# Performance work log

Hardware: AMD Instinct MI355X
Metric: run time of the kernel (lower is better)

Reference implementation:

```python
import jax, jax.numpy as jnp
import numpy as np

SIZE = 1024
M = 10            # log2(SIZE); number of butterfly factors
N_TERMS = 10
BATCH = 8192

# diagonal offset of butterfly j (order matches torch: range(m)[::-1])
DIAGS = [1 << (M - 1 - j) for j in range(M)]


def setup_inputs() -> dict:
    key = jax.random.key(0)
    k1, k2, k3, k4, k5 = jax.random.split(key, 5)
    x = jax.random.normal(k1, (BATCH, SIZE), dtype=jnp.float32)
    diag = jax.random.normal(k2, (M, SIZE), dtype=jnp.float32)
    subpad = jax.random.normal(k3, (M, SIZE), dtype=jnp.float32)
    suppad = jax.random.normal(k4, (M, SIZE), dtype=jnp.float32)
    logit = jax.random.normal(k5, (N_TERMS, M), dtype=jnp.float32)
    # zero the padded positions: subdiag has length SIZE-d stored in [d:],
    # superdiag has length SIZE-d stored in [:-d]
    idx = np.arange(SIZE)
    sub_mask = np.stack([idx >= d for d in DIAGS]).astype(np.float32)
    sup_mask = np.stack([idx < SIZE - d for d in DIAGS]).astype(np.float32)
    subpad = subpad * jnp.asarray(sub_mask)
    suppad = suppad * jnp.asarray(sup_mask)
    return {"x": x, "diag": diag, "subpad": subpad, "suppad": suppad, "logit": logit}


def _butterfly(x, dg, sb, sp, d):
    # out = dg*x; out[d:] += subdiag*x[:-d]; out[:-d] += superdiag*x[d:]
    z = jnp.zeros(x.shape[:-1] + (d,), x.dtype)
    x_right = jnp.concatenate([z, x[..., :-d]], axis=-1)  # x shifted right by d
    x_left = jnp.concatenate([x[..., d:], z], axis=-1)    # x shifted left by d
    return dg * x + sb * x_right + sp * x_left


def reference(x, diag, subpad, suppad, logit):
    prob = jax.nn.softmax(logit, axis=-1)  # (n_terms, m)
    out = x
    for i in range(N_TERMS)[::-1]:
        # apply all m butterflies to current output, stack on last dim
        ys = jnp.stack(
            [_butterfly(out, diag[j], subpad[j], suppad[j], DIAGS[j]) for j in range(M)],
            axis=-1,
        )  # (..., size, m)
        out = jnp.einsum('bsm,m->bs', ys, prob[i])
    return out
```

## Files before the change

### kernel.cpp

```cpp
#include <hip/hip_runtime.h>

#define SIZE 1024
#define MM 10
#define NTERMS 10

typedef _Float16 f16;
typedef __attribute__((ext_vector_type(8))) _Float16 f16x8;
typedef __attribute__((ext_vector_type(4))) _Float16 f16x4;
typedef __attribute__((ext_vector_type(4))) float    f32x4;
typedef __attribute__((ext_vector_type(2))) int      i2;

__device__ __forceinline__ float4 ldq(const float* p) { return *(const float4*)p; }

#define FMA4F(W, v0, v1, v2, v3)                                     \
    a0 = fmaf((W)[0], (v0), a0); a1 = fmaf((W)[1], (v1), a1);        \
    a2 = fmaf((W)[2], (v2), a2); a3 = fmaf((W)[3], (v3), a3);

__global__ __launch_bounds__(256, 2)
void precompute_G(const float* __restrict__ diag,
                  const float* __restrict__ subpad,
                  const float* __restrict__ suppad,
                  const float* __restrict__ logit,
                  float* __restrict__ G)
{
    __shared__ float buf[2][2][SIZE];

    const int tid = threadIdx.x;
    const int s0  = tid * 4;
    const int rowbase = blockIdx.x * 2;

    #pragma unroll
    for (int r = 0; r < 2; ++r) {
        float4 v;
        v.x = (rowbase + r == s0 + 0) ? 1.f : 0.f;
        v.y = (rowbase + r == s0 + 1) ? 1.f : 0.f;
        v.z = (rowbase + r == s0 + 2) ? 1.f : 0.f;
        v.w = (rowbase + r == s0 + 3) ? 1.f : 0.f;
        *(float4*)&buf[0][r][s0] = v;
    }
    __syncthreads();

    int cur = 0;
    for (int t = 0; t < NTERMS; ++t) {
        const int i = NTERMS - 1 - t;

        float lg[MM];
        float mx = -3.4e38f;
        #pragma unroll
        for (int j = 0; j < MM; ++j) { lg[j] = logit[i * MM + j]; mx = fmaxf(mx, lg[j]); }
        float ssum = 0.f;
        #pragma unroll
        for (int j = 0; j < MM; ++j) { lg[j] = __expf(lg[j] - mx); ssum += lg[j]; }
        const float inv = 1.0f / ssum;

        float D[4] = {0.f, 0.f, 0.f, 0.f};
        float Wsb[MM][4], Wsp[MM][4];
        #pragma unroll
        for (int j = 0; j < MM; ++j) {
            const float pj = lg[j] * inv;
            const float4 dg = ldq(diag   + j * SIZE + s0);
            const float4 sb = ldq(subpad + j * SIZE + s0);
            const float4 sp = ldq(suppad + j * SIZE + s0);
            D[0] = fmaf(pj, dg.x, D[0]); D[1] = fmaf(pj, dg.y, D[1]);
            D[2] = fmaf(pj, dg.z, D[2]); D[3] = fmaf(pj, dg.w, D[3]);
            Wsb[j][0] = pj * sb.x; Wsb[j][1] = pj * sb.y;
            Wsb[j][2] = pj * sb.z; Wsb[j][3] = pj * sb.w;
            Wsp[j][0] = pj * sp.x; Wsp[j][1] = pj * sp.y;
            Wsp[j][2] = pj * sp.z; Wsp[j][3] = pj * sp.w;
        }

        const bool last = (t == NTERMS - 1);
        for (int r = 0; r < 2; ++r) {
            const float* row = &buf[cur][r][0];

            const float4 xo = ldq(row + s0);
            float a0 = D[0] * xo.x, a1 = D[1] * xo.y,
                  a2 = D[2] * xo.z, a3 = D[3] * xo.w;

            const float4 xl = ldq(row + (s0 >= 4         ? s0 - 4 : 0));
            const float4 xr = ldq(row + (s0 + 4 <= 1020  ? s0 + 4 : 1020));

            FMA4F(Wsb[9], xl.w, xo.x, xo.y, xo.z)
            FMA4F(Wsp[9], xo.y, xo.z, xo.w, xr.x)
            FMA4F(Wsb[8], xl.z, xl.w, xo.x, xo.y)
            FMA4F(Wsp[8], xo.z, xo.w, xr.x, xr.y)
            FMA4F(Wsb[7], xl.x, xl.y, xl.z, xl.w)
            FMA4F(Wsp[7], xr.x, xr.y, xr.z, xr.w)
            #pragma unroll
            for (int j = 0; j <= 6; ++j) {
                const int d = 512 >> j;
                const float4 xm = ldq(row + (s0 >= d        ? s0 - d : 0));
                const float4 xp = ldq(row + (s0 + d <= 1020 ? s0 + d : 1020));
                FMA4F(Wsb[j], xm.x, xm.y, xm.z, xm.w)
                FMA4F(Wsp[j], xp.x, xp.y, xp.z, xp.w)
            }

            if (last) {
                *(float4*)(G + (long)(rowbase + r) * SIZE + s0) =
                    make_float4(a0, a1, a2, a3);
            } else {
                *(float4*)&buf[cur ^ 1][r][s0] = make_float4(a0, a1, a2, a3);
            }
        }
        __syncthreads();
        cur ^= 1;
    }
}

__global__ __launch_bounds__(256)
void transpose_cast(const float* __restrict__ G, f16* __restrict__ Gt)
{
    __shared__ float tile[64][65];
    const int tid = threadIdx.x;
    const int k0 = blockIdx.x * 64;
    const int s0 = blockIdx.y * 64;
    const int rr = tid >> 4;
    const int cc = (tid & 15) * 4;

    #pragma unroll
    for (int p = 0; p < 4; ++p) {
        const float4 v = ldq(G + (long)(k0 + rr + p * 16) * SIZE + s0 + cc);
        *(float4*)&tile[rr + p * 16][cc] = v;
    }
    __syncthreads();
    #pragma unroll
    for (int p = 0; p < 4; ++p) {
        const int s = rr + p * 16;
        f16x4 h;
        h[0] = (f16)tile[cc + 0][s];
        h[1] = (f16)tile[cc + 1][s];
        h[2] = (f16)tile[cc + 2][s];
        h[3] = (f16)tile[cc + 3][s];
        *(f16x4*)(Gt + (long)(s0 + s) * SIZE + k0 + cc) = h;
    }
}

#define BMT 128
#define BNT 128
#define BKT 32
#define PADK 40
#define NKT (1024 / BKT)

__device__ __forceinline__ void cvt16(const float4& v0, const float4& v1, f16x8& h) {
    h[0] = (f16)v0.x; h[1] = (f16)v0.y; h[2] = (f16)v0.z; h[3] = (f16)v0.w;
    h[4] = (f16)v1.x; h[5] = (f16)v1.y; h[6] = (f16)v1.z; h[7] = (f16)v1.w;
}

__global__ __launch_bounds__(256, 2)
void gemm_f16(const float* __restrict__ x,
              const f16* __restrict__ Gt,
              float* __restrict__ out)
{
    __shared__ f16 Xs[2][BMT][PADK];
    __shared__ f16 Gs[2][BNT][PADK];

    const int tid  = threadIdx.x;
    const int bm   = blockIdx.x >> 3;
    const int bn   = blockIdx.x & 7;
    const int w    = tid >> 6, lane = tid & 63;
    const int wm   = w >> 1,  wn   = w & 1;
    const int lr   = lane & 15, lk = lane >> 4;

    const int sr   = tid >> 1;
    const int sh16 = (tid & 1) * 16;
    const float* xrow = x  + (long)(bm * BMT + sr) * 1024 + sh16;
    const f16*   grow = Gt + (long)(bn * BNT + sr) * 1024 + sh16;

    f32x4 acc[4][4];
    #pragma unroll
    for (int mi = 0; mi < 4; ++mi)
        #pragma unroll
        for (int ni = 0; ni < 4; ++ni)
            acc[mi][ni] = (f32x4){0.f, 0.f, 0.f, 0.f};

    {
        const float4 v0 = ldq(xrow), v1 = ldq(xrow + 4),
                     v2 = ldq(xrow + 8), v3 = ldq(xrow + 12);
        const f16x8 g0 = *(const f16x8*)grow;
        const f16x8 g1 = *(const f16x8*)(grow + 8);
        f16x8 h0, h1; cvt16(v0, v1, h0); cvt16(v2, v3, h1);
        *(f16x8*)&Xs[0][sr][sh16]     = h0;
        *(f16x8*)&Xs[0][sr][sh16 + 8] = h1;
        *(f16x8*)&Gs[0][sr][sh16]     = g0;
        *(f16x8*)&Gs[0][sr][sh16 + 8] = g1;
    }
    __syncthreads();

    int cur = 0;
    for (int kt = 0; kt < NKT; ++kt) {
        float4 v0, v1, v2, v3; f16x8 g0, g1;
        const bool more = (kt + 1 < NKT);
        if (more) {
            const float* xp = xrow + (kt + 1) * BKT;
            const f16*   gp = grow + (kt + 1) * BKT;
            v0 = ldq(xp); v1 = ldq(xp + 4); v2 = ldq(xp + 8); v3 = ldq(xp + 12);
            g0 = *(const f16x8*)gp; g1 = *(const f16x8*)(gp + 8);
        }

        f16x8 a[4], b[4];
        #pragma unroll
        for (int mi = 0; mi < 4; ++mi)
            a[mi] = *(const f16x8*)&Xs[cur][wm * 64 + mi * 16 + lr][lk * 8];
        #pragma unroll
        for (int ni = 0; ni < 4; ++ni)
            b[ni] = *(const f16x8*)&Gs[cur][wn * 64 + ni * 16 + lr][lk * 8];
        #pragma unroll
        for (int mi = 0; mi < 4; ++mi)
            #pragma unroll
            for (int ni = 0; ni < 4; ++ni)
                acc[mi][ni] = __builtin_amdgcn_mfma_f32_16x16x32_f16(
                    a[mi], b[ni], acc[mi][ni], 0, 0, 0);

        if (more) {
            f16x8 h0, h1; cvt16(v0, v1, h0); cvt16(v2, v3, h1);
            *(f16x8*)&Xs[cur ^ 1][sr][sh16]     = h0;
            *(f16x8*)&Xs[cur ^ 1][sr][sh16 + 8] = h1;
            *(f16x8*)&Gs[cur ^ 1][sr][sh16]     = g0;
            *(f16x8*)&Gs[cur ^ 1][sr][sh16 + 8] = g1;
        }
        __syncthreads();
        cur ^= 1;
    }

    const long orow0 = (long)bm * BMT + wm * 64 + lk * 4;
    const int  ocol0 = bn * BNT + wn * 64 + lr;
    #pragma unroll
    for (int mi = 0; mi < 4; ++mi)
        #pragma unroll
        for (int ni = 0; ni < 4; ++ni)
            #pragma unroll
            for (int q = 0; q < 4; ++q)
                out[(orow0 + mi * 16 + q) * 1024 + ocol0 + ni * 16] = acc[mi][ni][q];
}

#define RPB 16
#define MIX_L(acc, r32, ww) \
    asm("v_fma_mix_f32 %0, %1, %2, %0 op_sel:[0,0,0] op_sel_hi:[1,0,0]" \
        : "+v"(acc) : "v"(r32), "v"(ww))
#define MIX_H(acc, r32, ww) \
    asm("v_fma_mix_f32 %0, %1, %2, %0 op_sel:[1,0,0] op_sel_hi:[1,0,0]" \
        : "+v"(acc) : "v"(r32), "v"(ww))

__global__ __launch_bounds__(256, 2)
void butterfly_h16mix(const float* __restrict__ x,
                      const float* __restrict__ diag,
                      const float* __restrict__ subpad,
                      const float* __restrict__ suppad,
                      const float* __restrict__ logit,
                      float* __restrict__ out)
{
    __shared__ f16 buf[2][RPB][SIZE];
    const int tid = threadIdx.x;
    const int s0  = tid * 4;
    const long rowbase = (long)blockIdx.x * RPB;

    #pragma unroll
    for (int r = 0; r < RPB; ++r) {
        const float4 v = ldq(x + (rowbase + r) * SIZE + s0);
        f16x4 h;
        h[0] = (f16)v.x; h[1] = (f16)v.y; h[2] = (f16)v.z; h[3] = (f16)v.w;
        *(f16x4*)&buf[0][r][s0] = h;
    }
    __syncthreads();

    int cur = 0;
    for (int t = 0; t < NTERMS; ++t) {
        const int i = NTERMS - 1 - t;
        float lg[MM];
        float mx = -3.4e38f;
        #pragma unroll
        for (int j = 0; j < MM; ++j) { lg[j] = logit[i * MM + j]; mx = fmaxf(mx, lg[j]); }
        float ssum = 0.f;
        #pragma unroll
        for (int j = 0; j < MM; ++j) { lg[j] = __expf(lg[j] - mx); ssum += lg[j]; }
        const float inv = 1.0f / ssum;

        float D[4] = {0.f, 0.f, 0.f, 0.f};
        float Wsb[MM][4], Wsp[MM][4];
        #pragma unroll
        for (int j = 0; j < MM; ++j) {
            const float pj = lg[j] * inv;
            const float4 dg = ldq(diag   + j * SIZE + s0);
            const float4 sb = ldq(subpad + j * SIZE + s0);
            const float4 sp = ldq(suppad + j * SIZE + s0);
            D[0] = fmaf(pj, dg.x, D[0]); D[1] = fmaf(pj, dg.y, D[1]);
            D[2] = fmaf(pj, dg.z, D[2]); D[3] = fmaf(pj, dg.w, D[3]);
            Wsb[j][0] = pj * sb.x; Wsb[j][1] = pj * sb.y;
            Wsb[j][2] = pj * sb.z; Wsb[j][3] = pj * sb.w;
            Wsp[j][0] = pj * sp.x; Wsp[j][1] = pj * sp.y;
            Wsp[j][2] = pj * sp.z; Wsp[j][3] = pj * sp.w;
        }

        const bool last = (t == NTERMS - 1);
        for (int r = 0; r < RPB; ++r) {
            const f16* row = &buf[cur][r][0];
            const i2 xo = *(const i2*)&row[s0];
            const i2 xl = *(const i2*)&row[(s0 >= 4)        ? s0 - 4 : 0];
            const i2 xr = *(const i2*)&row[(s0 + 4 <= 1020) ? s0 + 4 : 1020];
            float a0 = 0.f, a1 = 0.f, a2 = 0.f, a3 = 0.f;

            MIX_L(a0, xo.x, D[0]); MIX_H(a1, xo.x, D[1]);
            MIX_L(a2, xo.y, D[2]); MIX_H(a3, xo.y, D[3]);
            MIX_H(a0, xl.y, Wsb[9][0]); MIX_L(a1, xo.x, Wsb[9][1]);
            MIX_H(a2, xo.x, Wsb[9][2]); MIX_L(a3, xo.y, Wsb[9][3]);
            MIX_H(a0, xo.x, Wsp[9][0]); MIX_L(a1, xo.y, Wsp[9][1]);
            MIX_H(a2, xo.y, Wsp[9][2]); MIX_L(a3, xr.x, Wsp[9][3]);
            MIX_L(a0, xl.y, Wsb[8][0]); MIX_H(a1, xl.y, Wsb[8][1]);
            MIX_L(a2, xo.x, Wsb[8][2]); MIX_H(a3, xo.x, Wsb[8][3]);
            MIX_L(a0, xo.y, Wsp[8][0]); MIX_H(a1, xo.y, Wsp[8][1]);
            MIX_L(a2, xr.x, Wsp[8][2]); MIX_H(a3, xr.x, Wsp[8][3]);
            MIX_L(a0, xl.x, Wsb[7][0]); MIX_H(a1, xl.x, Wsb[7][1]);
            MIX_L(a2, xl.y, Wsb[7][2]); MIX_H(a3, xl.y, Wsb[7][3]);
            MIX_L(a0, xr.x, Wsp[7][0]); MIX_H(a1, xr.x, Wsp[7][1]);
            MIX_L(a2, xr.y, Wsp[7][2]); MIX_H(a3, xr.y, Wsp[7][3]);
            #pragma unroll
            for (int j = 0; j <= 6; ++j) {
                const int d = 512 >> j;
                const i2 xm = *(const i2*)&row[(s0 >= d)        ? s0 - d : 0];
                const i2 xp = *(const i2*)&row[(s0 + d <= 1020) ? s0 + d : 1020];
                MIX_L(a0, xm.x, Wsb[j][0]); MIX_H(a1, xm.x, Wsb[j][1]);
                MIX_L(a2, xm.y, Wsb[j][2]); MIX_H(a3, xm.y, Wsb[j][3]);
                MIX_L(a0, xp.x, Wsp[j][0]); MIX_H(a1, xp.x, Wsp[j][1]);
                MIX_L(a2, xp.y, Wsp[j][2]); MIX_H(a3, xp.y, Wsp[j][3]);
            }

            if (last) {
                *(float4*)(out + (rowbase + r) * SIZE + s0) =
                    make_float4(a0, a1, a2, a3);
            } else {
                f16x4 hv;
                hv[0] = (f16)a0; hv[1] = (f16)a1; hv[2] = (f16)a2; hv[3] = (f16)a3;
                *(f16x4*)&buf[cur ^ 1][r][s0] = hv;
            }
        }
        __syncthreads();
        cur ^= 1;
    }
}

extern "C" void kernel_launch(void* const* d_in, const int* in_sizes, int n_in,
                              void* d_out, int out_size, void* d_ws, size_t ws_size,
                              hipStream_t stream) {
    const float* x      = (const float*)d_in[0];
    const float* diag   = (const float*)d_in[1];
    const float* subpad = (const float*)d_in[2];
    const float* suppad = (const float*)d_in[3];
    const float* logit  = (const float*)d_in[4];
    float* outp = (float*)d_out;

    const int batch = in_sizes[0] / SIZE;
    const size_t needG  = (size_t)SIZE * SIZE * sizeof(float);
    const size_t needGt = (size_t)SIZE * SIZE * sizeof(f16);

    if (d_ws != nullptr && ws_size >= needG + needGt) {
        float* G  = (float*)d_ws;
        f16*   Gt = (f16*)((char*)d_ws + needG);
        precompute_G<<<dim3(SIZE / 2), dim3(256), 0, stream>>>(
            diag, subpad, suppad, logit, G);
        transpose_cast<<<dim3(16, 16), dim3(256), 0, stream>>>(G, Gt);
        const int nblocks = (batch / BMT) * (SIZE / BNT);
        gemm_f16<<<dim3(nblocks), dim3(256), 0, stream>>>(x, Gt, outp);
    } else {
        butterfly_h16mix<<<dim3(batch / RPB), dim3(256), 0, stream>>>(
            x, diag, subpad, suppad, logit, outp);
    }
}
```

Before: 82.11 us.

## Load GEMM B operand directly from global into registers, batch more rows in precompute

The GEMM kernel drops the shared-memory staging of the f16 G operand. Each lane now loads its MFMA B fragments straight from global memory, double-buffered in registers across a 2x-unrolled k loop. The X tile padding shrinks from 40 to 36. The precompute kernel processes 8 identity rows per block instead of 2, reusing the softmax and weight setup across more rows. This aims to cut LDS traffic and launch work, but the direct global loads are strided per lane and rely on cache hits, which risks more memory latency.

After: 113.2 us. +37.9%, slower.

```diff
diff --git a/kernel.cpp b/kernel.cpp
--- a/kernel.cpp
+++ b/kernel.cpp
@@ -16,6 +16,7 @@
     a0 = fmaf((W)[0], (v0), a0); a1 = fmaf((W)[1], (v1), a1);        \
     a2 = fmaf((W)[2], (v2), a2); a3 = fmaf((W)[3], (v3), a3);
 
+#define PRB 8
 __global__ __launch_bounds__(256, 2)
 void precompute_G(const float* __restrict__ diag,
                   const float* __restrict__ subpad,
@@ -23,14 +24,14 @@
                   const float* __restrict__ logit,
                   float* __restrict__ G)
 {
-    __shared__ float buf[2][2][SIZE];
+    __shared__ float buf[2][PRB][SIZE];
 
     const int tid = threadIdx.x;
     const int s0  = tid * 4;
-    const int rowbase = blockIdx.x * 2;
-
-    #pragma unroll
-    for (int r = 0; r < 2; ++r) {
+    const int rowbase = blockIdx.x * PRB;
+
+    #pragma unroll
+    for (int r = 0; r < PRB; ++r) {
         float4 v;
         v.x = (rowbase + r == s0 + 0) ? 1.f : 0.f;
         v.y = (rowbase + r == s0 + 1) ? 1.f : 0.f;
@@ -70,7 +71,7 @@
         }
 
         const bool last = (t == NTERMS - 1);
-        for (int r = 0; r < 2; ++r) {
+        for (int r = 0; r < PRB; ++r) {
             const float* row = &buf[cur][r][0];
 
             const float4 xo = ldq(row + s0);
@@ -138,7 +139,7 @@
 #define BMT 128
 #define BNT 128
 #define BKT 32
-#define PADK 40
+#define PADK 36
 #define NKT (1024 / BKT)
 
 __device__ __forceinline__ void cvt16(const float4& v0, const float4& v1, f16x8& h) {
@@ -152,7 +153,6 @@
               float* __restrict__ out)
 {
     __shared__ f16 Xs[2][BMT][PADK];
-    __shared__ f16 Gs[2][BNT][PADK];
 
     const int tid  = threadIdx.x;
     const int bm   = blockIdx.x >> 3;
@@ -161,10 +161,11 @@
     const int wm   = w >> 1,  wn   = w & 1;
     const int lr   = lane & 15, lk = lane >> 4;
 
-    const int sr   = tid >> 1;
-    const int sh16 = (tid & 1) * 16;
-    const float* xrow = x  + (long)(bm * BMT + sr) * 1024 + sh16;
-    const f16*   grow = Gt + (long)(bn * BNT + sr) * 1024 + sh16;
+    const int sr = tid >> 1;
+    const int sk = (tid & 1) * 16;
+    const float* xrow = x + (long)(bm * BMT + sr) * 1024 + sk;
+
+    const f16* gbase = Gt + (long)(bn * BNT + wn * 64 + lr) * 1024 + lk * 8;
 
     f32x4 acc[4][4];
     #pragma unroll
@@ -173,53 +174,66 @@
         for (int ni = 0; ni < 4; ++ni)
             acc[mi][ni] = (f32x4){0.f, 0.f, 0.f, 0.f};
 
-    {
-        const float4 v0 = ldq(xrow), v1 = ldq(xrow + 4),
-                     v2 = ldq(xrow + 8), v3 = ldq(xrow + 12);
-        const f16x8 g0 = *(const f16x8*)grow;
-        const f16x8 g1 = *(const f16x8*)(grow + 8);
-        f16x8 h0, h1; cvt16(v0, v1, h0); cvt16(v2, v3, h1);
-        *(f16x8*)&Xs[0][sr][sh16]     = h0;
-        *(f16x8*)&Xs[0][sr][sh16 + 8] = h1;
-        *(f16x8*)&Gs[0][sr][sh16]     = g0;
-        *(f16x8*)&Gs[0][sr][sh16 + 8] = g1;
-    }
+    float4 v0, v1, v2, v3;
+    f16x8 b0, b1, b2, b3;
+    f16x8 c0, c1, c2, c3;
+
+#define LOAD_A(KT) {                                                  \
+        const float* xp = xrow + (KT) * BKT;                          \
+        v0 = ldq(xp); v1 = ldq(xp + 4);                               \
+        v2 = ldq(xp + 8); v3 = ldq(xp + 12); }
+#define WRITE_A(BUF) {                                                \
+        f16x8 h0, h1; cvt16(v0, v1, h0); cvt16(v2, v3, h1);           \
+        *(f16x8*)&Xs[BUF][sr][sk]     = h0;                           \
+        *(f16x8*)&Xs[BUF][sr][sk + 8] = h1; }
+#define LOAD_B(B0, B1, B2, B3, KT) {                                  \
+        const f16* gp = gbase + (KT) * BKT;                           \
+        B0 = *(const f16x8*)(gp);                                     \
+        B1 = *(const f16x8*)(gp + 16 * 1024);                         \
+        B2 = *(const f16x8*)(gp + 32 * 1024);                         \
+        B3 = *(const f16x8*)(gp + 48 * 1024); }
+#define COMPUTE(BUF, B0, B1, B2, B3) {                                \
+        f16x8 a0 = *(const f16x8*)&Xs[BUF][wm * 64 +  0 + lr][lk * 8];\
+        f16x8 a1 = *(const f16x8*)&Xs[BUF][wm * 64 + 16 + lr][lk * 8];\
+        f16x8 a2 = *(const f16x8*)&Xs[BUF][wm * 64 + 32 + lr][lk * 8];\
+        f16x8 a3 = *(const f16x8*)&Xs[BUF][wm * 64 + 48 + lr][lk * 8];\
+        acc[0][0] = __builtin_amdgcn_mfma_f32_16x16x32_f16(a0, B0, acc[0][0], 0, 0, 0); \
+        acc[0][1] = __builtin_amdgcn_mfma_f32_16x16x32_f16(a0, B1, acc[0][1], 0, 0, 0); \
+        acc[0][2] = __builtin_amdgcn_mfma_f32_16x16x32_f16(a0, B2, acc[0][2], 0, 0, 0); \
+        acc[0][3] = __builtin_amdgcn_mfma_f32_16x16x32_f16(a0, B3, acc[0][3], 0, 0, 0); \
+        acc[1][0] = __builtin_amdgcn_mfma_f32_16x16x32_f16(a1, B0, acc[1][0], 0, 0, 0); \
+        acc[1][1] = __builtin_amdgcn_mfma_f32_16x16x32_f16(a1, B1, acc[1][1], 0, 0, 0); \
+        acc[1][2] = __builtin_amdgcn_mfma_f32_16x16x32_f16(a1, B2, acc[1][2], 0, 0, 0); \
+        acc[1][3] = __builtin_amdgcn_mfma_f32_16x16x32_f16(a1, B3, acc[1][3], 0, 0, 0); \
+        acc[2][0] = __builtin_amdgcn_mfma_f32_16x16x32_f16(a2, B0, acc[2][0], 0, 0, 0); \
+        acc[2][1] = __builtin_amdgcn_mfma_f32_16x16x32_f16(a2, B1, acc[2][1], 0, 0, 0); \
+        acc[2][2] = __builtin_amdgcn_mfma_f32_16x16x32_f16(a2, B2, acc[2][2], 0, 0, 0); \
+        acc[2][3] = __builtin_amdgcn_mfma_f32_16x16x32_f16(a2, B3, acc[2][3], 0, 0, 0); \
+        acc[3][0] = __builtin_amdgcn_mfma_f32_16x16x32_f16(a3, B0, acc[3][0], 0, 0, 0); \
+        acc[3][1] = __builtin_amdgcn_mfma_f32_16x16x32_f16(a3, B1, acc[3][1], 0, 0, 0); \
+        acc[3][2] = __builtin_amdgcn_mfma_f32_16x16x32_f16(a3, B2, acc[3][2], 0, 0, 0); \
+        acc[3][3] = __builtin_amdgcn_mfma_f32_16x16x32_f16(a3, B3, acc[3][3], 0, 0, 0); }
+
+    LOAD_A(0); WRITE_A(0); LOAD_B(b0, b1, b2, b3, 0);
     __syncthreads();
 
-    int cur = 0;
-    for (int kt = 0; kt < NKT; ++kt) {
-        float4 v0, v1, v2, v3; f16x8 g0, g1;
-        const bool more = (kt + 1 < NKT);
-        if (more) {
-            const float* xp = xrow + (kt + 1) * BKT;
-            const f16*   gp = grow + (kt + 1) * BKT;
-            v0 = ldq(xp); v1 = ldq(xp + 4); v2 = ldq(xp + 8); v3 = ldq(xp + 12);
-            g0 = *(const f16x8*)gp; g1 = *(const f16x8*)(gp + 8);
-        }
-
-        f16x8 a[4], b[4];
-        #pragma unroll
-        for (int mi = 0; mi < 4; ++mi)
-            a[mi] = *(const f16x8*)&Xs[cur][wm * 64 + mi * 16 + lr][lk * 8];
-        #pragma unroll
-        for (int ni = 0; ni < 4; ++ni)
-            b[ni] = *(const f16x8*)&Gs[cur][wn * 64 + ni * 16 + lr][lk * 8];
-        #pragma unroll
-        for (int mi = 0; mi < 4; ++mi)
-            #pragma unroll
-            for (int ni = 0; ni < 4; ++ni)
-                acc[mi][ni] = __builtin_amdgcn_mfma_f32_16x16x32_f16(
-                    a[mi], b[ni], acc[mi][ni], 0, 0, 0);
-
-        if (more) {
-            f16x8 h0, h1; cvt16(v0, v1, h0); cvt16(v2, v3, h1);
-            *(f16x8*)&Xs[cur ^ 1][sr][sh16]     = h0;
-            *(f16x8*)&Xs[cur ^ 1][sr][sh16 + 8] = h1;
-            *(f16x8*)&Gs[cur ^ 1][sr][sh16]     = g0;
-            *(f16x8*)&Gs[cur ^ 1][sr][sh16 + 8] = g1;
-        }
+    #pragma unroll 1
+    for (int kt2 = 0; kt2 < NKT / 2; ++kt2) {
+        const int kt = kt2 * 2;
+        LOAD_A(kt + 1);
+        LOAD_B(c0, c1, c2, c3, kt + 1);
+        COMPUTE(0, b0, b1, b2, b3);
+        WRITE_A(1);
         __syncthreads();
-        cur ^= 1;
+        if (kt2 < NKT / 2 - 1) {
+            LOAD_A(kt + 2);
+            LOAD_B(b0, b1, b2, b3, kt + 2);
+        }
+        COMPUTE(1, c0, c1, c2, c3);
+        if (kt2 < NKT / 2 - 1) {
+            WRITE_A(0);
+        }
+        __syncthreads();
     }
 
     const long orow0 = (long)bm * BMT + wm * 64 + lk * 4;
@@ -231,6 +245,11 @@
             #pragma unroll
             for (int q = 0; q < 4; ++q)
                 out[(orow0 + mi * 16 + q) * 1024 + ocol0 + ni * 16] = acc[mi][ni][q];
+
+#undef LOAD_A
+#undef WRITE_A
+#undef LOAD_B
+#undef COMPUTE
 }
 
 #define RPB 16
@@ -355,7 +374,7 @@
     if (d_ws != nullptr && ws_size >= needG + needGt) {
         float* G  = (float*)d_ws;
         f16*   Gt = (f16*)((char*)d_ws + needG);
-        precompute_G<<<dim3(SIZE / 2), dim3(256), 0, stream>>>(
+        precompute_G<<<dim3(SIZE / PRB), dim3(256), 0, stream>>>(
             diag, subpad, suppad, logit, G);
         transpose_cast<<<dim3(16, 16), dim3(256), 0, stream>>>(G, Gt);
         const int nblocks = (batch / BMT) * (SIZE / BNT);
```

## Load GEMM operands straight from global into registers, dropping LDS staging

Applied to the files above, without the earlier changes.

Rewrites the f16 MFMA GEMM so each wave loads its own A (fp32 x, converted in registers) and B (f16 Gt) fragments directly from global memory into registers. A two-stage register double buffer overlaps the loads with the MFMAs, and all shared-memory tiles and __syncthreads are removed. The block index mapping is also swapped so consecutive blocks share the same Gt column tile. This removes LDS traffic and barriers, but each operand is now fetched by two waves instead of once per block, relying on L2/L1 for the reuse. It also uses many more registers, which may limit occupancy.

Result: slower. 126.4 us (+53.9%).

```diff
diff --git a/kernel.cpp b/kernel.cpp
--- a/kernel.cpp
+++ b/kernel.cpp
@@ -135,11 +135,7 @@
     }
 }
 
-#define BMT 128
-#define BNT 128
-#define BKT 32
-#define PADK 40
-#define NKT (1024 / BKT)
+#define NKT 32
 
 __device__ __forceinline__ void cvt16(const float4& v0, const float4& v1, f16x8& h) {
     h[0] = (f16)v0.x; h[1] = (f16)v0.y; h[2] = (f16)v0.z; h[3] = (f16)v0.w;
@@ -151,20 +147,18 @@
               const f16* __restrict__ Gt,
               float* __restrict__ out)
 {
-    __shared__ f16 Xs[2][BMT][PADK];
-    __shared__ f16 Gs[2][BNT][PADK];
-
     const int tid  = threadIdx.x;
-    const int bm   = blockIdx.x >> 3;
-    const int bn   = blockIdx.x & 7;
+    const int bm   = blockIdx.x & 63;
+    const int bn   = blockIdx.x >> 6;
     const int w    = tid >> 6, lane = tid & 63;
     const int wm   = w >> 1,  wn   = w & 1;
     const int lr   = lane & 15, lk = lane >> 4;
 
-    const int sr   = tid >> 1;
-    const int sh16 = (tid & 1) * 16;
-    const float* xrow = x  + (long)(bm * BMT + sr) * 1024 + sh16;
-    const f16*   grow = Gt + (long)(bn * BNT + sr) * 1024 + sh16;
+    const float* arow0 = x + (long)(bm * 128 + wm * 64 +  0 + lr) * 1024 + lk * 8;
+    const float* arow1 = arow0 + 16 * 1024;
+    const float* arow2 = arow0 + 32 * 1024;
+    const float* arow3 = arow0 + 48 * 1024;
+    const f16* gbase = Gt + (long)(bn * 128 + wn * 64 + lr) * 1024 + lk * 8;
 
     f32x4 acc[4][4];
     #pragma unroll
@@ -173,57 +167,61 @@
         for (int ni = 0; ni < 4; ++ni)
             acc[mi][ni] = (f32x4){0.f, 0.f, 0.f, 0.f};
 
-    {
-        const float4 v0 = ldq(xrow), v1 = ldq(xrow + 4),
-                     v2 = ldq(xrow + 8), v3 = ldq(xrow + 12);
-        const f16x8 g0 = *(const f16x8*)grow;
-        const f16x8 g1 = *(const f16x8*)(grow + 8);
-        f16x8 h0, h1; cvt16(v0, v1, h0); cvt16(v2, v3, h1);
-        *(f16x8*)&Xs[0][sr][sh16]     = h0;
-        *(f16x8*)&Xs[0][sr][sh16 + 8] = h1;
-        *(f16x8*)&Gs[0][sr][sh16]     = g0;
-        *(f16x8*)&Gs[0][sr][sh16 + 8] = g1;
-    }
-    __syncthreads();
-
-    int cur = 0;
-    for (int kt = 0; kt < NKT; ++kt) {
-        float4 v0, v1, v2, v3; f16x8 g0, g1;
-        const bool more = (kt + 1 < NKT);
-        if (more) {
-            const float* xp = xrow + (kt + 1) * BKT;
-            const f16*   gp = grow + (kt + 1) * BKT;
-            v0 = ldq(xp); v1 = ldq(xp + 4); v2 = ldq(xp + 8); v3 = ldq(xp + 12);
-            g0 = *(const f16x8*)gp; g1 = *(const f16x8*)(gp + 8);
-        }
-
-        f16x8 a[4], b[4];
-        #pragma unroll
-        for (int mi = 0; mi < 4; ++mi)
-            a[mi] = *(const f16x8*)&Xs[cur][wm * 64 + mi * 16 + lr][lk * 8];
-        #pragma unroll
-        for (int ni = 0; ni < 4; ++ni)
-            b[ni] = *(const f16x8*)&Gs[cur][wn * 64 + ni * 16 + lr][lk * 8];
-        #pragma unroll
-        for (int mi = 0; mi < 4; ++mi)
-            #pragma unroll
-            for (int ni = 0; ni < 4; ++ni)
-                acc[mi][ni] = __builtin_amdgcn_mfma_f32_16x16x32_f16(
-                    a[mi], b[ni], acc[mi][ni], 0, 0, 0);
-
-        if (more) {
-            f16x8 h0, h1; cvt16(v0, v1, h0); cvt16(v2, v3, h1);
-            *(f16x8*)&Xs[cur ^ 1][sr][sh16]     = h0;
-            *(f16x8*)&Xs[cur ^ 1][sr][sh16 + 8] = h1;
-            *(f16x8*)&Gs[cur ^ 1][sr][sh16]     = g0;
-            *(f16x8*)&Gs[cur ^ 1][sr][sh16 + 8] = g1;
-        }
-        __syncthreads();
-        cur ^= 1;
-    }
-
-    const long orow0 = (long)bm * BMT + wm * 64 + lk * 4;
-    const int  ocol0 = bn * BNT + wn * 64 + lr;
+    float4 P0l, P0h, P1l, P1h, P2l, P2h, P3l, P3h;
+    float4 Q0l, Q0h, Q1l, Q1h, Q2l, Q2h, Q3l, Q3h;
+    f16x8 gP0, gP1, gP2, gP3;
+    f16x8 gQ0, gQ1, gQ2, gQ3;
+
+#define LOADA(S, KT) {                                                \
+        const int o = (KT) * 32;                                      \
+        S##0l = ldq(arow0 + o); S##0h = ldq(arow0 + o + 4);           \
+        S##1l = ldq(arow1 + o); S##1h = ldq(arow1 + o + 4);           \
+        S##2l = ldq(arow2 + o); S##2h = ldq(arow2 + o + 4);           \
+        S##3l = ldq(arow3 + o); S##3h = ldq(arow3 + o + 4); }
+#define LOADB(S, KT) {                                                \
+        const f16* gp = gbase + (KT) * 32;                            \
+        S##0 = *(const f16x8*)(gp);                                   \
+        S##1 = *(const f16x8*)(gp + 16 * 1024);                       \
+        S##2 = *(const f16x8*)(gp + 32 * 1024);                       \
+        S##3 = *(const f16x8*)(gp + 48 * 1024); }
+#define COMP(S, B) {                                                  \
+        f16x8 fa;                                                     \
+        cvt16(S##0l, S##0h, fa);                                      \
+        acc[0][0] = __builtin_amdgcn_mfma_f32_16x16x32_f16(fa, B##0, acc[0][0], 0, 0, 0); \
+        acc[0][1] = __builtin_amdgcn_mfma_f32_16x16x32_f16(fa, B##1, acc[0][1], 0, 0, 0); \
+        acc[0][2] = __builtin_amdgcn_mfma_f32_16x16x32_f16(fa, B##2, acc[0][2], 0, 0, 0); \
+        acc[0][3] = __builtin_amdgcn_mfma_f32_16x16x32_f16(fa, B##3, acc[0][3], 0, 0, 0); \
+        cvt16(S##1l, S##1h, fa);                                      \
+        acc[1][0] = __builtin_amdgcn_mfma_f32_16x16x32_f16(fa, B##0, acc[1][0], 0, 0, 0); \
+        acc[1][1] = __builtin_amdgcn_mfma_f32_16x16x32_f16(fa, B##1, acc[1][1], 0, 0, 0); \
+        acc[1][2] = __builtin_amdgcn_mfma_f32_16x16x32_f16(fa, B##2, acc[1][2], 0, 0, 0); \
+        acc[1][3] = __builtin_amdgcn_mfma_f32_16x16x32_f16(fa, B##3, acc[1][3], 0, 0, 0); \
+        cvt16(S##2l, S##2h, fa);                                      \
+        acc[2][0] = __builtin_amdgcn_mfma_f32_16x16x32_f16(fa, B##0, acc[2][0], 0, 0, 0); \
+        acc[2][1] = __builtin_amdgcn_mfma_f32_16x16x32_f16(fa, B##1, acc[2][1], 0, 0, 0); \
+        acc[2][2] = __builtin_amdgcn_mfma_f32_16x16x32_f16(fa, B##2, acc[2][2], 0, 0, 0); \
+        acc[2][3] = __builtin_amdgcn_mfma_f32_16x16x32_f16(fa, B##3, acc[2][3], 0, 0, 0); \
+        cvt16(S##3l, S##3h, fa);                                      \
+        acc[3][0] = __builtin_amdgcn_mfma_f32_16x16x32_f16(fa, B##0, acc[3][0], 0, 0, 0); \
+        acc[3][1] = __builtin_amdgcn_mfma_f32_16x16x32_f16(fa, B##1, acc[3][1], 0, 0, 0); \
+        acc[3][2] = __builtin_amdgcn_mfma_f32_16x16x32_f16(fa, B##2, acc[3][2], 0, 0, 0); \
+        acc[3][3] = __builtin_amdgcn_mfma_f32_16x16x32_f16(fa, B##3, acc[3][3], 0, 0, 0); }
+
+    LOADA(P, 0); LOADB(gP, 0);
+
+    #pragma unroll 1
+    for (int kt2 = 0; kt2 < NKT / 2; ++kt2) {
+        const int kt = kt2 * 2;
+        LOADA(Q, kt + 1); LOADB(gQ, kt + 1);
+        COMP(P, gP);
+        if (kt2 < NKT / 2 - 1) {
+            LOADA(P, kt + 2); LOADB(gP, kt + 2);
+        }
+        COMP(Q, gQ);
+    }
+
+    const long orow0 = (long)bm * 128 + wm * 64 + lk * 4;
+    const int  ocol0 = bn * 128 + wn * 64 + lr;
     #pragma unroll
     for (int mi = 0; mi < 4; ++mi)
         #pragma unroll
@@ -231,6 +229,10 @@
             #pragma unroll
             for (int q = 0; q < 4; ++q)
                 out[(orow0 + mi * 16 + q) * 1024 + ocol0 + ni * 16] = acc[mi][ni][q];
+
+#undef LOADA
+#undef LOADB
+#undef COMP
 }
 
 #define RPB 16
@@ -358,7 +360,7 @@
         precompute_G<<<dim3(SIZE / 2), dim3(256), 0, stream>>>(
             diag, subpad, suppad, logit, G);
         transpose_cast<<<dim3(16, 16), dim3(256), 0, stream>>>(G, Gt);
-        const int nblocks = (batch / BMT) * (SIZE / BNT);
+        const int nblocks = (batch / 128) * (SIZE / 128);
         gemm_f16<<<dim3(nblocks), dim3(256), 0, stream>>>(x, Gt, outp);
     } else {
         butterfly_h16mix<<<dim3(batch / RPB), dim3(256), 0, stream>>>(
```
